# Kernel optimization log

Hardware: AMD Instinct MI355X
Metric: run time of the kernel (lower is better)

The kernel has to match this reference:

```python
import jax, jax.numpy as jnp
import numpy as np

D_MODEL = 1024
D_HEAD = 64

def setup_inputs() -> dict:
    key = jax.random.key(0)
    ks = jax.random.split(key, 7)
    s = 1.0 / np.sqrt(D_MODEL)
    x = jax.random.normal(ks[0], (4, 4096, D_MODEL), dtype=jnp.float32)
    Wq = jax.random.uniform(ks[1], (D_MODEL, D_HEAD), jnp.float32, -s, s)
    bq = jax.random.uniform(ks[2], (D_HEAD,), jnp.float32, -s, s)
    Wk = jax.random.uniform(ks[3], (D_MODEL, D_HEAD), jnp.float32, -s, s)
    bk = jax.random.uniform(ks[4], (D_HEAD,), jnp.float32, -s, s)
    Wv = jax.random.uniform(ks[5], (D_MODEL, D_HEAD), jnp.float32, -s, s)
    bv = jax.random.uniform(ks[6], (D_HEAD,), jnp.float32, -s, s)
    return {"x": x, "Wq": Wq, "bq": bq, "Wk": Wk, "bk": bk, "Wv": Wv, "bv": bv}

def reference(x, Wq, bq, Wk, bk, Wv, bv):
    # x: [b, s, d_model] -> Q,K,V: [b, s, d_head]
    Q = jnp.einsum('bsd,dh->bsh', x, Wq) + bq
    K = jnp.einsum('bsd,dh->bsh', x, Wk) + bk
    V = jnp.einsum('bsd,dh->bsh', x, Wv) + bv
    scale = 1.0 / jnp.sqrt(jnp.asarray(D_HEAD, x.dtype))
    scores = jnp.einsum('bqh,bkh->bqk', Q, K) * scale  # [b, s, s]
    attn = jax.nn.softmax(scores, axis=-1)
    return jnp.einsum('bqk,bkh->bqh', attn, V)  # [b, s, d_head]
```

## Files before the change

kernel.cpp:

```cpp
#include <hip/hip_runtime.h>

typedef __bf16 bf16x8 __attribute__((ext_vector_type(8)));
typedef __bf16 bf16x4 __attribute__((ext_vector_type(4)));
typedef float f32x4 __attribute__((ext_vector_type(4)));
typedef unsigned short u16x8 __attribute__((ext_vector_type(8)));

union FragU { u16x8 u; bf16x8 b; };
union PackU { bf16x4 v; unsigned long long q; };

__device__ __forceinline__ unsigned short bfbits(float f) {
  __bf16 h = (__bf16)f;
  union { __bf16 h; unsigned short s; } cv; cv.h = h;
  return cv.s;
}

#define MFMA16(a, b, c) __builtin_amdgcn_mfma_f32_16x16x32_bf16((a), (b), (c), 0, 0, 0)

#define QSCALE 0.18033688011112042f

__global__ __launch_bounds__(256) void wt_kernel(
    const float* __restrict__ Wq, const float* __restrict__ Wk, const float* __restrict__ Wv,
    unsigned short* __restrict__ WF)
{
  const int m = blockIdx.x >> 5;
  const int c = blockIdx.x & 31;
  const float* W = (m == 0) ? Wq : ((m == 1) ? Wk : Wv);
  const int t = threadIdx.x >> 6;
  const int lane = threadIdx.x & 63;
  const int l15 = lane & 15;
  const int g = lane >> 4;
  unsigned short* dst = WF + ((((size_t)m * 32 + c) * 4 + t) * 64 + lane) * 8;
#pragma unroll
  for (int e = 0; e < 8; ++e)
    dst[e] = bfbits(W[(size_t)(32 * c + 8 * g + e) * 64 + (16 * t + l15)]);
}

__global__ __launch_bounds__(256, 1) void proj_kernel(
    const float* __restrict__ x, const unsigned short* __restrict__ WF,
    const float* __restrict__ bq, const float* __restrict__ bk, const float* __restrict__ bv,
    unsigned short* __restrict__ Qb, unsigned short* __restrict__ KF,
    unsigned short* __restrict__ VF)
{
  __shared__ __align__(16) unsigned short ldsW[2][3][8192];
  const int tid = threadIdx.x;
  const int lane = tid & 63;
  const int wid = tid >> 6;
  const int l15 = lane & 15;
  const int g = lane >> 4;
  const int row0 = blockIdx.x * 64 + wid * 16;

  f32x4 accQ[4], accK[4], accV[4];
  const f32x4 zero = {0.f, 0.f, 0.f, 0.f};
#pragma unroll
  for (int i = 0; i < 4; ++i) { accQ[i] = zero; accK[i] = zero; accV[i] = zero; }

  const float* xrow = x + (size_t)(row0 + l15) * 1024;

  f32x4 xx0[4], xx1[4];
  u16x8 stW[3][4];

#define WLD(W0) { _Pragma("unroll") for (int m_ = 0; m_ < 3; ++m_) \
  _Pragma("unroll") for (int i_ = 0; i_ < 4; ++i_) \
    stW[m_][i_] = *(const u16x8*)(WF + (size_t)(m_ * 32 + (W0) * 4) * 2048 + \
                                  wid * 2048 + i_ * 512 + lane * 8); }

#define WWR(P) { _Pragma("unroll") for (int m_ = 0; m_ < 3; ++m_) \
  _Pragma("unroll") for (int i_ = 0; i_ < 4; ++i_) \
    *(u16x8*)&ldsW[P][m_][wid * 2048 + i_ * 512 + lane * 8] = stW[m_][i_]; }

#define PLDX(XB, C) { xx0[XB] = *(const f32x4*)(xrow + 32 * (C) + 8 * g); \
                      xx1[XB] = *(const f32x4*)(xrow + 32 * (C) + 8 * g + 4); }

#define PHALFL(P, CW, XB, CXN) { \
    FragU xf; \
    _Pragma("unroll") for (int i_ = 0; i_ < 4; ++i_) { \
      xf.b[i_] = (__bf16)xx0[XB][i_]; xf.b[4 + i_] = (__bf16)xx1[XB][i_]; } \
    if ((CXN) < 32) PLDX(XB, CXN); \
    _Pragma("unroll") for (int t = 0; t < 4; ++t) { \
      const bf16x8 wq_ = *(const bf16x8*)&ldsW[P][0][((CW) * 4 + t) * 512 + lane * 8]; \
      const bf16x8 wk_ = *(const bf16x8*)&ldsW[P][1][((CW) * 4 + t) * 512 + lane * 8]; \
      const bf16x8 wv_ = *(const bf16x8*)&ldsW[P][2][((CW) * 4 + t) * 512 + lane * 8]; \
      accQ[t] = MFMA16(xf.b, wq_, accQ[t]); \
      accK[t] = MFMA16(xf.b, wk_, accK[t]); \
      accV[t] = MFMA16(wv_, xf.b, accV[t]); } }

  WLD(0) WWR(0) WLD(1)
  PLDX(0, 0) PLDX(1, 1) PLDX(2, 2) PLDX(3, 3)

#pragma unroll 1
  for (int w0 = 0; w0 < 8; ++w0) {
    const int p = w0 & 1;
    __syncthreads();
    if (w0 < 7) WWR(p ^ 1)
    if (w0 < 6) WLD(w0 + 2)
    const int c = w0 * 4;
    PHALFL(p, 0, 0, c + 4)
    PHALFL(p, 1, 1, c + 5)
    PHALFL(p, 2, 2, c + 6)
    PHALFL(p, 3, 3, c + 7)
  }

  const int b = blockIdx.x >> 6;
  const int kt = blockIdx.x & 63;
  const int q0 = row0 & 4095;
  unsigned short* Qbase = Qb + (size_t)b * 4096 * 64;
#pragma unroll
  for (int t = 0; t < 4; ++t) {
    const int hh = 16 * t + l15;
    const float bqv = bq[hh];
#pragma unroll
    for (int r = 0; r < 4; ++r)
      Qbase[(size_t)(q0 + 4 * g + r) * 64 + hh] = bfbits((accQ[t][r] + bqv) * QSCALE);
  }
  unsigned short* KFb = KF + ((size_t)b * 64 + kt) * 4096;
  unsigned short* VFb = VF + ((size_t)b * 64 + kt) * 4096;
#pragma unroll
  for (int t = 0; t < 4; ++t) {
    const int hh = 16 * t + l15;
    const float bkv = bk[hh];
#pragma unroll
    for (int r = 0; r < 4; ++r) {
      KFb[(size_t)((wid * 2 + (t >> 1)) * 64 + (t & 1) * 32 + (l15 >> 3) * 16 + 4 * g + r) * 8 +
          (l15 & 7)] = bfbits(accK[t][r] + bkv);
      const int hv = 16 * t + 4 * g + r;
      VFb[(size_t)((t * 2 + (wid >> 1)) * 64 + (wid & 1) * 32 + (l15 >> 3) * 16 + 4 * g + r) * 8 +
          (l15 & 7)] = bfbits(accV[t][r] + bv[hv]);
    }
  }
}

__global__ __launch_bounds__(256, 2) void flash_kernel(
    const unsigned short* __restrict__ Qb, const unsigned short* __restrict__ KF,
    const unsigned short* __restrict__ VF, float* __restrict__ out)
{
  __shared__ __align__(16) unsigned char lds[36864];
  const int tid = threadIdx.x;
  const int lane = tid & 63;
  const int w = tid >> 6;
  const int l15 = lane & 15;
  const int g = lane >> 4;
  const int bid = blockIdx.x;
  const int xcd = bid & 7;
  const int b = xcd >> 1;
  const int qt = (bid >> 3) * 2 + (xcd & 1);
  const int q0 = qt * 32;

  const unsigned short* Qp = Qb + (size_t)b * 4096 * 64;
  const unsigned short* KFb = KF + (size_t)b * 262144;
  const unsigned short* VFb = VF + (size_t)b * 262144;

  const bf16x8 qfA0 = *(const bf16x8*)(Qp + (size_t)(q0 + l15) * 64 + 8 * g);
  const bf16x8 qfA1 = *(const bf16x8*)(Qp + (size_t)(q0 + l15) * 64 + 32 + 8 * g);
  const bf16x8 qfB0 = *(const bf16x8*)(Qp + (size_t)(q0 + 16 + l15) * 64 + 8 * g);
  const bf16x8 qfB1 = *(const bf16x8*)(Qp + (size_t)(q0 + 16 + l15) * 64 + 32 + 8 * g);

  f32x4 O_A[4], O_B[4];
  const f32x4 zero = {0.f, 0.f, 0.f, 0.f};
#pragma unroll
  for (int i = 0; i < 4; ++i) { O_A[i] = zero; O_B[i] = zero; }
  float mA = -INFINITY, lA = 0.f, mB = -INFINITY, lB = 0.f;
  unsigned short* PwA = (unsigned short*)lds + (w * 2 + 0) * 1152;
  unsigned short* PwB = (unsigned short*)lds + (w * 2 + 1) * 1152;

#define SM_HALF(S, mvar, lvar, OA, PW) { \
  float mt = fmaxf(fmaxf(S[0][0], S[0][1]), fmaxf(S[0][2], S[0][3])); \
  _Pragma("unroll") for (int t = 1; t < 4; ++t) \
    _Pragma("unroll") for (int r = 0; r < 4; ++r) mt = fmaxf(mt, S[t][r]); \
  mt = fmaxf(mt, __shfl_xor(mt, 16)); \
  mt = fmaxf(mt, __shfl_xor(mt, 32)); \
  if (!__all(mt <= mvar + 8.0f)) { \
    const float mnew = fmaxf(mvar, mt); \
    const float alpha = __builtin_amdgcn_exp2f(mvar - mnew); \
    mvar = mnew; lvar *= alpha; \
    _Pragma("unroll") for (int r = 0; r < 4; ++r) { \
      const float ar = __shfl(alpha, 4 * g + r); \
      OA[0][r] *= ar; OA[1][r] *= ar; OA[2][r] *= ar; OA[3][r] *= ar; } \
  } \
  float ps = 0.f; \
  _Pragma("unroll") for (int t = 0; t < 4; ++t) { \
    const float p0 = __builtin_amdgcn_exp2f(S[t][0] - mvar); \
    const float p1 = __builtin_amdgcn_exp2f(S[t][1] - mvar); \
    const float p2 = __builtin_amdgcn_exp2f(S[t][2] - mvar); \
    const float p3 = __builtin_amdgcn_exp2f(S[t][3] - mvar); \
    ps += (p0 + p1) + (p2 + p3); \
    PackU pk_; pk_.v[0] = (__bf16)p0; pk_.v[1] = (__bf16)p1; \
    pk_.v[2] = (__bf16)p2; pk_.v[3] = (__bf16)p3; \
    *(unsigned long long*)((PW) + l15 * 72 + 16 * t + 4 * g) = pk_.q; } \
  ps += __shfl_xor(ps, 16); \
  ps += __shfl_xor(ps, 32); \
  lvar += ps; }

#pragma unroll 1
  for (int kt = w; kt < 64; kt += 4) {
    const unsigned short* Kt = KFb + kt * 4096;
    const unsigned short* Vt = VFb + kt * 4096;
    bf16x8 kf[8], vf[8];
#pragma unroll
    for (int j = 0; j < 8; ++j) kf[j] = *(const bf16x8*)(Kt + (j * 64 + lane) * 8);
#pragma unroll
    for (int j = 0; j < 8; ++j) vf[j] = *(const bf16x8*)(Vt + (j * 64 + lane) * 8);
    f32x4 S_A[4], S_B[4];
#pragma unroll
    for (int t = 0; t < 4; ++t) {
      S_A[t] = zero;
      S_A[t] = MFMA16(kf[2 * t], qfA0, S_A[t]);
      S_A[t] = MFMA16(kf[2 * t + 1], qfA1, S_A[t]);
      S_B[t] = zero;
      S_B[t] = MFMA16(kf[2 * t], qfB0, S_B[t]);
      S_B[t] = MFMA16(kf[2 * t + 1], qfB1, S_B[t]);
    }
    SM_HALF(S_A, mA, lA, O_A, PwA)
    SM_HALF(S_B, mB, lB, O_B, PwB)
#pragma unroll
    for (int s = 0; s < 2; ++s) {
      const bf16x8 paA = *(const bf16x8*)(PwA + l15 * 72 + 32 * s + 8 * g);
      const bf16x8 paB = *(const bf16x8*)(PwB + l15 * 72 + 32 * s + 8 * g);
#pragma unroll
      for (int nt = 0; nt < 4; ++nt) {
        O_A[nt] = MFMA16(paA, vf[2 * nt + s], O_A[nt]);
        O_B[nt] = MFMA16(paB, vf[2 * nt + s], O_B[nt]);
      }
    }
  }

  __syncthreads();
  float* O_l = (float*)lds;
  float* mlp = (float*)(lds + 34816);
#pragma unroll
  for (int nt = 0; nt < 4; ++nt)
#pragma unroll
    for (int r = 0; r < 4; ++r) {
      O_l[((w * 2 + 0) * 16 + 4 * g + r) * 68 + 16 * nt + l15] = O_A[nt][r];
      O_l[((w * 2 + 1) * 16 + 4 * g + r) * 68 + 16 * nt + l15] = O_B[nt][r];
    }
  if (g == 0) {
    mlp[((w * 2 + 0) * 16 + l15) * 2] = mA; mlp[((w * 2 + 0) * 16 + l15) * 2 + 1] = lA;
    mlp[((w * 2 + 1) * 16 + l15) * 2] = mB; mlp[((w * 2 + 1) * 16 + l15) * 2 + 1] = lB;
  }
  __syncthreads();

  const int q = tid >> 3;
  const int h0 = (tid & 7) * 8;
  const int qh = q >> 4, qr = q & 15;
  float M = -INFINITY;
#pragma unroll
  for (int s = 0; s < 4; ++s) M = fmaxf(M, mlp[((s * 2 + qh) * 16 + qr) * 2]);
  float L = 0.f;
  f32x4 a0 = zero, a1 = zero;
#pragma unroll
  for (int s = 0; s < 4; ++s) {
    const int rowi = (s * 2 + qh) * 16 + qr;
    const float wgt = __builtin_amdgcn_exp2f(mlp[rowi * 2] - M);
    L += wgt * mlp[rowi * 2 + 1];
    const f32x4 o0 = *(const f32x4*)&O_l[rowi * 68 + h0];
    const f32x4 o1 = *(const f32x4*)&O_l[rowi * 68 + h0 + 4];
#pragma unroll
    for (int i = 0; i < 4; ++i) { a0[i] += wgt * o0[i]; a1[i] += wgt * o1[i]; }
  }
  const float inv = 1.0f / L;
  float* ob = out + ((size_t)b * 4096 + qt * 32 + q) * 64 + h0;
  f32x4 r0 = {a0[0] * inv, a0[1] * inv, a0[2] * inv, a0[3] * inv};
  f32x4 r1 = {a1[0] * inv, a1[1] * inv, a1[2] * inv, a1[3] * inv};
  *(f32x4*)ob = r0;
  *(f32x4*)(ob + 4) = r1;
}

extern "C" void kernel_launch(void* const* d_in, const int* in_sizes, int n_in,
                              void* d_out, int out_size, void* d_ws, size_t ws_size,
                              hipStream_t stream) {
  const float* x  = (const float*)d_in[0];
  const float* Wq = (const float*)d_in[1];
  const float* bq = (const float*)d_in[2];
  const float* Wk = (const float*)d_in[3];
  const float* bk = (const float*)d_in[4];
  const float* Wv = (const float*)d_in[5];
  const float* bv = (const float*)d_in[6];

  char* ws = (char*)d_ws;
  unsigned short* WF = (unsigned short*)ws;
  unsigned short* Qb = (unsigned short*)(ws + (512u << 10));
  unsigned short* KF = (unsigned short*)(ws + (512u << 10) + (2u << 20));
  unsigned short* VF = (unsigned short*)(ws + (512u << 10) + (4u << 20));
  float* out = (float*)d_out;

  hipLaunchKernelGGL(wt_kernel,    dim3(96),  dim3(256), 0, stream, Wq, Wk, Wv, WF);
  hipLaunchKernelGGL(proj_kernel,  dim3(256), dim3(256), 0, stream, x, WF, bq, bk, bv, Qb, KF, VF);
  hipLaunchKernelGGL(flash_kernel, dim3(512), dim3(256), 0, stream, Qb, KF, VF, out);
}
```

Before: 59.37 us.

## Stream projection weights into LDS via direct global-to-LDS loads with 4-stage ring

Replaces the register-staged weight double buffer (global load into registers, then LDS write) with __builtin_amdgcn_global_load_lds, which copies weight chunks straight into a 4-slot LDS ring three chunks ahead. Synchronisation becomes a barrier per 32-wide k chunk, with explicit vmcnt waits tuned to the number of outstanding loads. The aim is to drop the VGPR staging and LDS write instructions and keep more loads in flight. In exchange it adds a barrier per chunk instead of per four chunks, and the hand-counted waitcnt values must stay correct.

After: 56.25 us. -5.3%, faster.

```diff
diff --git a/kernel.cpp b/kernel.cpp
--- a/kernel.cpp
+++ b/kernel.cpp
@@ -41,7 +41,7 @@
     unsigned short* __restrict__ Qb, unsigned short* __restrict__ KF,
     unsigned short* __restrict__ VF)
 {
-  __shared__ __align__(16) unsigned short ldsW[2][3][8192];
+  __shared__ __align__(16) unsigned short ldsW[4][6144];
   const int tid = threadIdx.x;
   const int lane = tid & 63;
   const int wid = tid >> 6;
@@ -55,50 +55,53 @@
   for (int i = 0; i < 4; ++i) { accQ[i] = zero; accK[i] = zero; accV[i] = zero; }
 
   const float* xrow = x + (size_t)(row0 + l15) * 1024;
-
   f32x4 xx0[4], xx1[4];
-  u16x8 stW[3][4];
-
-#define WLD(W0) { _Pragma("unroll") for (int m_ = 0; m_ < 3; ++m_) \
-  _Pragma("unroll") for (int i_ = 0; i_ < 4; ++i_) \
-    stW[m_][i_] = *(const u16x8*)(WF + (size_t)(m_ * 32 + (W0) * 4) * 2048 + \
-                                  wid * 2048 + i_ * 512 + lane * 8); }
-
-#define WWR(P) { _Pragma("unroll") for (int m_ = 0; m_ < 3; ++m_) \
-  _Pragma("unroll") for (int i_ = 0; i_ < 4; ++i_) \
-    *(u16x8*)&ldsW[P][m_][wid * 2048 + i_ * 512 + lane * 8] = stW[m_][i_]; }
+
+#define WDMA(CC) { const int sl_ = (CC) & 3; \
+    _Pragma("unroll") for (int m_ = 0; m_ < 3; ++m_) { \
+      const unsigned short* gs_ = WF + ((((size_t)m_ * 32 + (CC)) * 4 + wid) * 64 + lane) * 8; \
+      __builtin_amdgcn_global_load_lds( \
+          (const __attribute__((address_space(1))) void*)gs_, \
+          (__attribute__((address_space(3))) void*)&ldsW[sl_][(m_ * 4 + wid) * 512], \
+          16, 0, 0); } }
 
 #define PLDX(XB, C) { xx0[XB] = *(const f32x4*)(xrow + 32 * (C) + 8 * g); \
                       xx1[XB] = *(const f32x4*)(xrow + 32 * (C) + 8 * g + 4); }
 
-#define PHALFL(P, CW, XB, CXN) { \
+#define SUBIT(CC, KK, WIMM, DOW, DOX) { \
+    asm volatile("s_waitcnt vmcnt(" #WIMM ")" ::: "memory"); \
+    __builtin_amdgcn_s_barrier(); \
+    __builtin_amdgcn_sched_barrier(0); \
+    if (DOW) WDMA((CC) + 3); \
     FragU xf; \
     _Pragma("unroll") for (int i_ = 0; i_ < 4; ++i_) { \
-      xf.b[i_] = (__bf16)xx0[XB][i_]; xf.b[4 + i_] = (__bf16)xx1[XB][i_]; } \
-    if ((CXN) < 32) PLDX(XB, CXN); \
-    _Pragma("unroll") for (int t = 0; t < 4; ++t) { \
-      const bf16x8 wq_ = *(const bf16x8*)&ldsW[P][0][((CW) * 4 + t) * 512 + lane * 8]; \
-      const bf16x8 wk_ = *(const bf16x8*)&ldsW[P][1][((CW) * 4 + t) * 512 + lane * 8]; \
-      const bf16x8 wv_ = *(const bf16x8*)&ldsW[P][2][((CW) * 4 + t) * 512 + lane * 8]; \
-      accQ[t] = MFMA16(xf.b, wq_, accQ[t]); \
-      accK[t] = MFMA16(xf.b, wk_, accK[t]); \
-      accV[t] = MFMA16(wv_, xf.b, accV[t]); } }
-
-  WLD(0) WWR(0) WLD(1)
+      xf.b[i_] = (__bf16)xx0[KK][i_]; xf.b[4 + i_] = (__bf16)xx1[KK][i_]; } \
+    if (DOX) PLDX(KK, (CC) + 4); \
+    { const int rs_ = (CC) & 3; \
+      _Pragma("unroll") for (int t = 0; t < 4; ++t) { \
+        const bf16x8 wq_ = *(const bf16x8*)&ldsW[rs_][(0 * 4 + t) * 512 + lane * 8]; \
+        const bf16x8 wk_ = *(const bf16x8*)&ldsW[rs_][(1 * 4 + t) * 512 + lane * 8]; \
+        const bf16x8 wv_ = *(const bf16x8*)&ldsW[rs_][(2 * 4 + t) * 512 + lane * 8]; \
+        accQ[t] = MFMA16(xf.b, wq_, accQ[t]); \
+        accK[t] = MFMA16(xf.b, wk_, accK[t]); \
+        accV[t] = MFMA16(wv_, xf.b, accV[t]); } } }
+
+  WDMA(0)
+  __builtin_amdgcn_sched_barrier(0);
+  WDMA(1) WDMA(2)
   PLDX(0, 0) PLDX(1, 1) PLDX(2, 2) PLDX(3, 3)
 
 #pragma unroll 1
-  for (int w0 = 0; w0 < 8; ++w0) {
-    const int p = w0 & 1;
-    __syncthreads();
-    if (w0 < 7) WWR(p ^ 1)
-    if (w0 < 6) WLD(w0 + 2)
-    const int c = w0 * 4;
-    PHALFL(p, 0, 0, c + 4)
-    PHALFL(p, 1, 1, c + 5)
-    PHALFL(p, 2, 2, c + 6)
-    PHALFL(p, 3, 3, c + 7)
-  }
+  for (int cb = 0; cb < 28; cb += 4) {
+    SUBIT(cb + 0, 0, 10, 1, 1)
+    SUBIT(cb + 1, 1, 10, 1, 1)
+    SUBIT(cb + 2, 2, 10, 1, 1)
+    SUBIT(cb + 3, 3, 10, 1, 1)
+  }
+  SUBIT(28, 0, 10, 1, 0)
+  SUBIT(29, 1, 8, 0, 0)
+  SUBIT(30, 2, 3, 0, 0)
+  SUBIT(31, 3, 0, 0, 0)
 
   const int b = blockIdx.x >> 6;
   const int kt = blockIdx.x & 63;
```
